# Kernel tuning notes

Measured on AMD Instinct MI355X. Metric: run time of the kernel, lower is better.

The kernel has to match this reference:

```python
import jax, jax.numpy as jnp
import numpy as np

B, S, IK, IV = 16, 2048, 3, 1
D = IK + IV          # input_size = 4
H = 256              # hidden_size
F = 512              # dim_feedforward
L = 2                # num_layers
EPS = 1e-5


def setup_inputs() -> dict:
    key = jax.random.key(0)
    ks = jax.random.split(key, 16)
    n = jax.random.normal
    inp = {
        'KEY': n(ks[0], (B, S, IK), jnp.float32),
        'VALUE': n(ks[1], (B, S, IV), jnp.float32),
        # per-layer kernel-attention projections (stacked on layer axis)
        'Wq': n(ks[2], (L, D, H), jnp.float32) * 0.1,
        'bq': jnp.zeros((L, H), jnp.float32),
        'Wk': n(ks[3], (L, D, H), jnp.float32) * 0.1,
        'bk': jnp.zeros((L, H), jnp.float32),
        'Wv': n(ks[4], (L, D, H), jnp.float32) * 0.1,
        'bv': jnp.zeros((L, H), jnp.float32),
        'Wo': n(ks[5], (L, H, D), jnp.float32) * 0.1,
        'bo': jnp.zeros((L, D), jnp.float32),
        'bw': jnp.ones((L,), jnp.float32),          # Gaussian kernel bandwidth
        # LayerNorm 1
        'g1': jnp.ones((L, D), jnp.float32),
        'be1': jnp.zeros((L, D), jnp.float32),
        # FFN
        'W1': n(ks[6], (L, D, F), jnp.float32) * 0.1,
        'b1': jnp.zeros((L, F), jnp.float32),
        'W2': n(ks[7], (L, F, D), jnp.float32) * 0.1,
        'b2': jnp.zeros((L, D), jnp.float32),
        # LayerNorm 2
        'g2': jnp.ones((L, D), jnp.float32),
        'be2': jnp.zeros((L, D), jnp.float32),
        # final fc: input_size -> input_v
        'Wfc': n(ks[8], (D, IV), jnp.float32) * 0.1,
        'bfc': jnp.zeros((IV,), jnp.float32),
    }
    return inp


def _layernorm(x, g, b):
    m = x.mean(-1, keepdims=True)
    v = ((x - m) ** 2).mean(-1, keepdims=True)
    return (x - m) * jax.lax.rsqrt(v + EPS) * g + b


def reference(KEY, VALUE, Wq, bq, Wk, bk, Wv, bv, Wo, bo, bw,
              g1, be1, W1, b1, W2, b2, g2, be2, Wfc, bfc):
    # positioning: concat coords and values -> [B, S, D]
    X = jnp.concatenate([KEY, VALUE], axis=-1)
    n_layers = Wq.shape[0]
    for i in range(n_layers):
        # Nadaraya-Watson Gaussian kernel attention (madsnn, type='nwd', kernel='gauss')
        Q = X @ Wq[i] + bq[i]                      # [B,S,H]
        K = X @ Wk[i] + bk[i]                      # [B,S,H]
        V = X @ Wv[i] + bv[i]                      # [B,S,H]
        # pairwise squared distances ||q-k||^2, [B,S,S]
        d2 = ((Q * Q).sum(-1)[:, :, None]
              + (K * K).sum(-1)[:, None, :]
              - 2.0 * jnp.einsum('bqh,bkh->bqk', Q, K))
        attn = jax.nn.softmax(-0.5 * d2 * (bw[i] ** 2), axis=-1)
        attn_out = jnp.einsum('bqk,bkh->bqh', attn, V) @ Wo[i] + bo[i]  # [B,S,D]
        # residual + LayerNorm + FFN + residual + LayerNorm (dropout = identity in eval)
        res = _layernorm(X + attn_out, g1[i], be1[i])
        ff = jax.nn.relu(res @ W1[i] + b1[i]) @ W2[i] + b2[i]
        X = _layernorm(res + ff, g2[i], be2[i])
    return X @ Wfc + bfc                            # [B,S,IV]
```

## Files before the change

### kernel.cpp

```cpp
#include <hip/hip_runtime.h>

#define BB 16
#define SS 2048
#define NTOK (BB*SS)
#define FF 512
#define EPSF 1e-5f

#if __has_builtin(__builtin_amdgcn_exp2f)
#define EXP2F(x) __builtin_amdgcn_exp2f(x)
#else
#define EXP2F(x) exp2f(x)
#endif

typedef float v2f __attribute__((ext_vector_type(2)));


__device__ __forceinline__ float wred64(float v) {
#pragma unroll
  for (int m = 32; m > 0; m >>= 1) v += __shfl_xor(v, m, 64);
  return v;
}


__global__ __launch_bounds__(256) void prep_kernel(
    const float* __restrict__ KEY, const float* __restrict__ VALUE,
    const float* __restrict__ Wq, const float* __restrict__ bq,
    const float* __restrict__ Wk, const float* __restrict__ bk,
    const float* __restrict__ Wv, const float* __restrict__ bv,
    const float* __restrict__ Wo, const float* __restrict__ bw,
    const float* __restrict__ W1, const float* __restrict__ b1,
    const float* __restrict__ W2,
    float* __restrict__ sm, float* __restrict__ w1t, float* __restrict__ X0)
{
  const int bid = blockIdx.x;
  if (bid < 128) {
    const int gq = bid*256 + threadIdx.x;
    *(float4*)(X0 + (size_t)gq*4) =
        make_float4(KEY[gq*3 + 0], KEY[gq*3 + 1], KEY[gq*3 + 2], VALUE[gq]);
    return;
  }
  const int i = bid - 128;
  if (threadIdx.x >= 64) return;
  const int lane = threadIdx.x;
  float m4[4][4] = {{0}}, gkk[4][4] = {{0}}, wvo[4][4] = {{0}};
  float akk[4] = {0}, bvo[4] = {0};
  float ck1 = 0.f, ck2 = 0.f;

  for (int h = lane; h < 256; h += 64) {
    float vq[4], vk[4], vv[4], wo4[4];
#pragma unroll
    for (int a = 0; a < 4; ++a) {
      vq[a]  = Wq[(i*4 + a)*256 + h];
      vk[a]  = Wk[(i*4 + a)*256 + h];
      vv[a]  = Wv[(i*4 + a)*256 + h];
      wo4[a] = Wo[(i*256 + h)*4 + a];
    }
    const float bqh = bq[i*256 + h], bkh = bk[i*256 + h], bvh = bv[i*256 + h];
#pragma unroll
    for (int a = 0; a < 4; ++a) {
#pragma unroll
      for (int c = 0; c < 4; ++c) {
        m4[a][c]  = fmaf(vq[a], vk[c], m4[a][c]);
        gkk[a][c] = fmaf(vk[a], vk[c], gkk[a][c]);
        wvo[a][c] = fmaf(vv[a], wo4[c], wvo[a][c]);
      }
      akk[a] = fmaf(vk[a], bqh - bkh, akk[a]);
      bvo[a] = fmaf(bvh, wo4[a], bvo[a]);
    }
    ck1 = fmaf(bqh, bkh, ck1);
    ck2 = fmaf(bkh, bkh, ck2);
  }
#pragma unroll
  for (int a = 0; a < 4; ++a) {
#pragma unroll
    for (int c = 0; c < 4; ++c) {
      m4[a][c]  = wred64(m4[a][c]);
      gkk[a][c] = wred64(gkk[a][c]);
      wvo[a][c] = wred64(wvo[a][c]);
    }
    akk[a] = wred64(akk[a]);
    bvo[a] = wred64(bvo[a]);
  }
  ck1 = wred64(ck1); ck2 = wred64(ck2);

  if (lane == 0) {
    const float bwv = bw[i];
    const float bw2 = bwv * bwv * 1.44269504088896f;
    float* s = sm + i*64;
#pragma unroll
    for (int a = 0; a < 4; ++a) {
#pragma unroll
      for (int c = 0; c < 4; ++c) {
        s[a*4+c]      = bw2 * m4[a][c];
        s[16 + a*4+c] = -0.5f * bw2 * gkk[a][c];
        s[32 + a*4+c] = wvo[a][c];
      }
      s[48+a] = bw2 * akk[a];
      s[52+a] = bvo[a];
    }
    s[56] = bw2 * (ck1 - 0.5f * ck2);
  }
  for (int f = lane; f < FF; f += 64) {
    float* rec = w1t + (i*FF + f)*12;
#pragma unroll
    for (int c = 0; c < 4; ++c) rec[c]   = W1[(i*4 + c)*FF + f];
#pragma unroll
    for (int c = 0; c < 4; ++c) rec[4+c] = W2[(i*FF + f)*4 + c];
    rec[8] = b1[i*FF + f];
    rec[9] = 0.f; rec[10] = 0.f; rec[11] = 0.f;
  }
}

__device__ __forceinline__ void compute_feat(const float x[4], const float* __restrict__ s,
                                             float* __restrict__ featrec)
{
  float P[4], VT[4], tk[4];
#pragma unroll
  for (int a = 0; a < 4; ++a) {
    P[a]  = fmaf(s[a*4+3], x[3], fmaf(s[a*4+2], x[2], fmaf(s[a*4+1], x[1], s[a*4+0]*x[0])));
    tk[a] = fmaf(s[16+a*4+3], x[3], fmaf(s[16+a*4+2], x[2], fmaf(s[16+a*4+1], x[1], s[16+a*4+0]*x[0])));
    VT[a] = s[52+a] + fmaf(s[32+3*4+a], x[3], fmaf(s[32+2*4+a], x[2], fmaf(s[32+1*4+a], x[1], s[32+0*4+a]*x[0])));
  }
  float R = s[56];
#pragma unroll
  for (int a = 0; a < 4; ++a) R = fmaf(tk[a] + s[48+a], x[a], R);
  float4* fp = (float4*)featrec;
  fp[0] = make_float4(P[0], P[1], P[2], P[3]);
  fp[1] = make_float4(VT[0], VT[1], VT[2], VT[3]);
  fp[2] = make_float4(R, 0.f, 0.f, 0.f);
}

__global__ __launch_bounds__(256) void attn_kernel(
    const float* __restrict__ X, const float* __restrict__ sm,
    float* __restrict__ part)
{
  __shared__ float smem[512*21];
  const int bid = blockIdx.x;
  const int b = bid >> 5;
  const int r = bid & 31;
  const int qg = r >> 3, kb = r & 7;
  const int qbase = (b << 11) + (qg << 9);
  const int kbase = (b << 11) + (kb << 8);
  const int tid = threadIdx.x;
  const int lane = tid & 63, wave = tid >> 6;

  {
    const float4 xk = *(const float4*)(X + (size_t)(kbase + tid)*4);
    float xr[4] = {xk.x, xk.y, xk.z, xk.w};
    float fr[12];
    compute_feat(xr, sm, fr);
    float* dst = smem + tid*12;
    ((float4*)dst)[0] = ((float4*)fr)[0];
    ((float4*)dst)[1] = ((float4*)fr)[1];
    dst[8] = fr[8];
  }

  v2f xq2[4][4], axy[8], azw[8], ad[4];
#pragma unroll
  for (int jp = 0; jp < 4; ++jp) {
    const float4 xa = *(const float4*)(X + (size_t)(qbase + (2*jp  )*64 + lane)*4);
    const float4 xb = *(const float4*)(X + (size_t)(qbase + (2*jp+1)*64 + lane)*4);
    xq2[jp][0] = v2f{xa.x, xb.x};
    xq2[jp][1] = v2f{xa.y, xb.y};
    xq2[jp][2] = v2f{xa.z, xb.z};
    xq2[jp][3] = v2f{xa.w, xb.w};
    ad[jp] = v2f{0.f, 0.f};
  }
#pragma unroll
  for (int j = 0; j < 8; ++j) { axy[j] = v2f{0.f, 0.f}; azw[j] = v2f{0.f, 0.f}; }
  __syncthreads();

  const float* kf = smem + wave*64*12;
#pragma unroll 2
  for (int k = 0; k < 64; ++k) {
    const float* kp = kf + k*12;
    const float4 P  = *(const float4*)kp;
    const float4 VT = *(const float4*)(kp + 4);
    const float R = kp[8];
    const v2f Rv  = v2f{R, R};
    const v2f Px  = v2f{P.x, P.x}, Py = v2f{P.y, P.y};
    const v2f Pz  = v2f{P.z, P.z}, Pw = v2f{P.w, P.w};
    const v2f Vxy = v2f{VT.x, VT.y}, Vzw = v2f{VT.z, VT.w};
#pragma unroll
    for (int jp = 0; jp < 4; ++jp) {
      v2f l = __builtin_elementwise_fma(xq2[jp][0], Px, Rv);
      l = __builtin_elementwise_fma(xq2[jp][1], Py, l);
      l = __builtin_elementwise_fma(xq2[jp][2], Pz, l);
      l = __builtin_elementwise_fma(xq2[jp][3], Pw, l);
      const float e0 = EXP2F(l.x);
      const float e1 = EXP2F(l.y);
      const v2f e0v = v2f{e0, e0}, e1v = v2f{e1, e1};
      axy[2*jp  ] = __builtin_elementwise_fma(e0v, Vxy, axy[2*jp  ]);
      azw[2*jp  ] = __builtin_elementwise_fma(e0v, Vzw, azw[2*jp  ]);
      axy[2*jp+1] = __builtin_elementwise_fma(e1v, Vxy, axy[2*jp+1]);
      azw[2*jp+1] = __builtin_elementwise_fma(e1v, Vzw, azw[2*jp+1]);
      ad[jp] += v2f{e0, e1};
    }
  }
  __syncthreads();
#pragma unroll
  for (int j = 0; j < 8; ++j) {
    float* rr = smem + (j*64 + lane)*21 + wave*5;
    rr[0] = axy[j].x; rr[1] = axy[j].y; rr[2] = azw[j].x;
    rr[3] = azw[j].y; rr[4] = (j & 1) ? ad[j>>1].y : ad[j>>1].x;
  }
  __syncthreads();
  float* pb = part + (size_t)kb * NTOK * 8;
#pragma unroll
  for (int t = 0; t < 2; ++t) {
    const int q = t*256 + tid;
    const float* rr = smem + q*21;
    float s0 = 0.f, s1 = 0.f, s2 = 0.f, s3 = 0.f, s4 = 0.f;
#pragma unroll
    for (int w = 0; w < 4; ++w) {
      s0 += rr[w*5+0]; s1 += rr[w*5+1]; s2 += rr[w*5+2];
      s3 += rr[w*5+3]; s4 += rr[w*5+4];
    }
    float* pp = pb + (size_t)(qbase + q)*8;
    *(float4*)pp = make_float4(s0, s1, s2, s3);
    pp[4] = s4;
  }
}

__device__ __forceinline__ void ln4(const float t[4], const float* __restrict__ g,
                                    const float* __restrict__ b, float r[4])
{
  const float m = 0.25f*(t[0]+t[1]+t[2]+t[3]);
  const float d0 = t[0]-m, d1 = t[1]-m, d2 = t[2]-m, d3 = t[3]-m;
  const float v = 0.25f*(d0*d0 + d1*d1 + d2*d2 + d3*d3);
  const float sc = rsqrtf(v + EPSF);
  r[0] = fmaf(d0*sc, g[0], b[0]);
  r[1] = fmaf(d1*sc, g[1], b[1]);
  r[2] = fmaf(d2*sc, g[2], b[2]);
  r[3] = fmaf(d3*sc, g[3], b[3]);
}

__global__ __launch_bounds__(512) void combine_kernel(
    const float* __restrict__ part, const float* __restrict__ Xin,
    const float* __restrict__ w1t,
    const float* __restrict__ bo, const float* __restrict__ g1, const float* __restrict__ be1,
    const float* __restrict__ b2v, const float* __restrict__ g2, const float* __restrict__ be2,
    float* __restrict__ Xout,
    const float* __restrict__ Wfc, const float* __restrict__ bfc,
    float* __restrict__ outp, int last)
{
  const int tok = threadIdx.x & 63, fc = threadIdx.x >> 6;
  const int gq = blockIdx.x*64 + tok;
  __shared__ float redp[8][64][5];
  __shared__ float ress[64][4];
  __shared__ float redf[8][64][4];

  {
    const float* pp = part + ((size_t)fc*NTOK + gq)*8;
    const float4 v = *(const float4*)pp;
    redp[fc][tok][0] = v.x; redp[fc][tok][1] = v.y;
    redp[fc][tok][2] = v.z; redp[fc][tok][3] = v.w;
    redp[fc][tok][4] = pp[4];
  }
  __syncthreads();

  if (fc == 0) {
    float acc[5] = {0,0,0,0,0};
#pragma unroll
    for (int k = 0; k < 8; ++k)
#pragma unroll
      for (int c = 0; c < 5; ++c) acc[c] += redp[k][tok][c];
    const float inv = 1.0f / acc[4];
    const float4 xv = *(const float4*)(Xin + (size_t)gq*4);
    float t[4];
    t[0] = xv.x + fmaf(acc[0], inv, bo[0]);
    t[1] = xv.y + fmaf(acc[1], inv, bo[1]);
    t[2] = xv.z + fmaf(acc[2], inv, bo[2]);
    t[3] = xv.w + fmaf(acc[3], inv, bo[3]);
    float r[4];
    ln4(t, g1, be1, r);
    ress[tok][0] = r[0]; ress[tok][1] = r[1]; ress[tok][2] = r[2]; ress[tok][3] = r[3];
  }
  __syncthreads();

  const float r0 = ress[tok][0], r1 = ress[tok][1], r2 = ress[tok][2], r3 = ress[tok][3];
  float fa[4] = {0,0,0,0};
  const float* wt = w1t + (size_t)fc*64*12;
#pragma unroll 4
  for (int f = 0; f < 64; ++f) {
    const float* rec = wt + f*12;
    const float4 w1r = *(const float4*)rec;
    const float4 w2r = *(const float4*)(rec + 4);
    const float b1f = rec[8];
    float h = fmaf(r3, w1r.w, fmaf(r2, w1r.z, fmaf(r1, w1r.y, fmaf(r0, w1r.x, b1f))));
    h = fmaxf(h, 0.f);
    fa[0] = fmaf(h, w2r.x, fa[0]);
    fa[1] = fmaf(h, w2r.y, fa[1]);
    fa[2] = fmaf(h, w2r.z, fa[2]);
    fa[3] = fmaf(h, w2r.w, fa[3]);
  }
  redf[fc][tok][0] = fa[0]; redf[fc][tok][1] = fa[1];
  redf[fc][tok][2] = fa[2]; redf[fc][tok][3] = fa[3];
  __syncthreads();

  if (fc == 0) {
    float t2[4];
#pragma unroll
    for (int c = 0; c < 4; ++c) {
      float s = b2v[c];
#pragma unroll
      for (int k = 0; k < 8; ++k) s += redf[k][tok][c];
      t2[c] = ress[tok][c] + s;
    }
    float y[4];
    ln4(t2, g2, be2, y);
    if (last) {
      outp[gq] = fmaf(y[3], Wfc[3], fmaf(y[2], Wfc[2], fmaf(y[1], Wfc[1], fmaf(y[0], Wfc[0], bfc[0]))));
    } else {
      *(float4*)(Xout + (size_t)gq*4) = make_float4(y[0], y[1], y[2], y[3]);
    }
  }
}

extern "C" void kernel_launch(void* const* d_in, const int* in_sizes, int n_in,
                              void* d_out, int out_size, void* d_ws, size_t ws_size,
                              hipStream_t stream)
{
  const float* KEY   = (const float*)d_in[0];
  const float* VALUE = (const float*)d_in[1];
  const float* Wq  = (const float*)d_in[2];
  const float* bq  = (const float*)d_in[3];
  const float* Wk  = (const float*)d_in[4];
  const float* bk  = (const float*)d_in[5];
  const float* Wv  = (const float*)d_in[6];
  const float* bv  = (const float*)d_in[7];
  const float* Wo  = (const float*)d_in[8];
  const float* bo  = (const float*)d_in[9];
  const float* bw  = (const float*)d_in[10];
  const float* g1  = (const float*)d_in[11];
  const float* be1 = (const float*)d_in[12];
  const float* W1  = (const float*)d_in[13];
  const float* b1  = (const float*)d_in[14];
  const float* W2  = (const float*)d_in[15];
  const float* b2  = (const float*)d_in[16];
  const float* g2  = (const float*)d_in[17];
  const float* be2 = (const float*)d_in[18];
  const float* Wfc = (const float*)d_in[19];
  const float* bfc = (const float*)d_in[20];
  float* out = (float*)d_out;

  float* w    = (float*)d_ws;
  float* sm   = w;
  float* w1t  = w + 128;
  float* X0   = w + 12416;
  float* X1   = w + 143488;
  float* part = w + 274560;

  prep_kernel<<<130, 256, 0, stream>>>(KEY, VALUE, Wq, bq, Wk, bk, Wv, bv, Wo, bw,
                                       W1, b1, W2, sm, w1t, X0);

  attn_kernel<<<512, 256, 0, stream>>>(X0, sm, part);
  combine_kernel<<<512, 512, 0, stream>>>(part, X0, w1t,
      bo, g1, be1, b2, g2, be2,
      X1, Wfc, bfc, out, 0);

  attn_kernel<<<512, 256, 0, stream>>>(X1, sm + 64, part);
  combine_kernel<<<512, 512, 0, stream>>>(part, X1, w1t + FF*12,
      bo + 4, g1 + 4, be1 + 4, b2 + 4, g2 + 4, be2 + 4,
      X0, Wfc, bfc, out, 1);
}
```

Baseline: 182.5 us.

## Halve attention query tile per block and pack FFN weights for paired-float math

The attention kernel now handles 256 queries per block instead of 512, doubling the grid to 1024 blocks and halving per-thread accumulator registers. Key features are now computed twice as often across blocks. Separately, the FFN weights are repacked into 24-float records covering two hidden units, so the combine kernel can run the FFN with packed two-wide FMAs. The aims are higher occupancy and better load balance in attention, and fewer instructions in the FFN loop.

Measured after the change: 184.1 us. No clear change (+0.9%).

```diff
diff --git a/kernel.cpp b/kernel.cpp
--- a/kernel.cpp
+++ b/kernel.cpp
@@ -100,14 +100,20 @@
     }
     s[56] = bw2 * (ck1 - 0.5f * ck2);
   }
-  for (int f = lane; f < FF; f += 64) {
-    float* rec = w1t + (i*FF + f)*12;
-#pragma unroll
-    for (int c = 0; c < 4; ++c) rec[c]   = W1[(i*4 + c)*FF + f];
-#pragma unroll
-    for (int c = 0; c < 4; ++c) rec[4+c] = W2[(i*FF + f)*4 + c];
-    rec[8] = b1[i*FF + f];
-    rec[9] = 0.f; rec[10] = 0.f; rec[11] = 0.f;
+  for (int fp = lane; fp < 256; fp += 64) {
+    const int f0 = 2*fp, f1 = 2*fp + 1;
+    float* rec = w1t + (i*256 + fp)*24;
+#pragma unroll
+    for (int c = 0; c < 4; ++c) {
+      rec[c*2 + 0] = W1[(i*4 + c)*FF + f0];
+      rec[c*2 + 1] = W1[(i*4 + c)*FF + f1];
+      rec[8 + c*2 + 0] = W2[((size_t)i*FF + f0)*4 + c];
+      rec[8 + c*2 + 1] = W2[((size_t)i*FF + f1)*4 + c];
+    }
+    rec[16] = b1[i*FF + f0];
+    rec[17] = b1[i*FF + f1];
+#pragma unroll
+    for (int c = 18; c < 24; ++c) rec[c] = 0.f;
   }
 }
 
@@ -134,12 +140,12 @@
     const float* __restrict__ X, const float* __restrict__ sm,
     float* __restrict__ part)
 {
-  __shared__ float smem[512*21];
+  __shared__ float smem[256*21];
   const int bid = blockIdx.x;
-  const int b = bid >> 5;
-  const int r = bid & 31;
+  const int b = bid >> 6;
+  const int r = bid & 63;
   const int qg = r >> 3, kb = r & 7;
-  const int qbase = (b << 11) + (qg << 9);
+  const int qbase = (b << 11) + (qg << 8);
   const int kbase = (b << 11) + (kb << 8);
   const int tid = threadIdx.x;
   const int lane = tid & 63, wave = tid >> 6;
@@ -155,9 +161,9 @@
     dst[8] = fr[8];
   }
 
-  v2f xq2[4][4], axy[8], azw[8], ad[4];
-#pragma unroll
-  for (int jp = 0; jp < 4; ++jp) {
+  v2f xq2[2][4], axy[4], azw[4], ad[2];
+#pragma unroll
+  for (int jp = 0; jp < 2; ++jp) {
     const float4 xa = *(const float4*)(X + (size_t)(qbase + (2*jp  )*64 + lane)*4);
     const float4 xb = *(const float4*)(X + (size_t)(qbase + (2*jp+1)*64 + lane)*4);
     xq2[jp][0] = v2f{xa.x, xb.x};
@@ -167,7 +173,7 @@
     ad[jp] = v2f{0.f, 0.f};
   }
 #pragma unroll
-  for (int j = 0; j < 8; ++j) { axy[j] = v2f{0.f, 0.f}; azw[j] = v2f{0.f, 0.f}; }
+  for (int j = 0; j < 4; ++j) { axy[j] = v2f{0.f, 0.f}; azw[j] = v2f{0.f, 0.f}; }
   __syncthreads();
 
   const float* kf = smem + wave*64*12;
@@ -182,7 +188,7 @@
     const v2f Pz  = v2f{P.z, P.z}, Pw = v2f{P.w, P.w};
     const v2f Vxy = v2f{VT.x, VT.y}, Vzw = v2f{VT.z, VT.w};
 #pragma unroll
-    for (int jp = 0; jp < 4; ++jp) {
+    for (int jp = 0; jp < 2; ++jp) {
       v2f l = __builtin_elementwise_fma(xq2[jp][0], Px, Rv);
       l = __builtin_elementwise_fma(xq2[jp][1], Py, l);
       l = __builtin_elementwise_fma(xq2[jp][2], Pz, l);
@@ -199,24 +205,21 @@
   }
   __syncthreads();
 #pragma unroll
-  for (int j = 0; j < 8; ++j) {
+  for (int j = 0; j < 4; ++j) {
     float* rr = smem + (j*64 + lane)*21 + wave*5;
     rr[0] = axy[j].x; rr[1] = axy[j].y; rr[2] = azw[j].x;
     rr[3] = azw[j].y; rr[4] = (j & 1) ? ad[j>>1].y : ad[j>>1].x;
   }
   __syncthreads();
-  float* pb = part + (size_t)kb * NTOK * 8;
-#pragma unroll
-  for (int t = 0; t < 2; ++t) {
-    const int q = t*256 + tid;
-    const float* rr = smem + q*21;
+  {
+    const float* rr = smem + tid*21;
     float s0 = 0.f, s1 = 0.f, s2 = 0.f, s3 = 0.f, s4 = 0.f;
 #pragma unroll
     for (int w = 0; w < 4; ++w) {
       s0 += rr[w*5+0]; s1 += rr[w*5+1]; s2 += rr[w*5+2];
       s3 += rr[w*5+3]; s4 += rr[w*5+4];
     }
-    float* pp = pb + (size_t)(qbase + q)*8;
+    float* pp = part + ((size_t)kb * NTOK + qbase + tid)*8;
     *(float4*)pp = make_float4(s0, s1, s2, s3);
     pp[4] = s4;
   }
@@ -278,24 +281,36 @@
   }
   __syncthreads();
 
-  const float r0 = ress[tok][0], r1 = ress[tok][1], r2 = ress[tok][2], r3 = ress[tok][3];
-  float fa[4] = {0,0,0,0};
-  const float* wt = w1t + (size_t)fc*64*12;
+  const v2f r0v = v2f{ress[tok][0], ress[tok][0]};
+  const v2f r1v = v2f{ress[tok][1], ress[tok][1]};
+  const v2f r2v = v2f{ress[tok][2], ress[tok][2]};
+  const v2f r3v = v2f{ress[tok][3], ress[tok][3]};
+  v2f f2[4];
+#pragma unroll
+  for (int c = 0; c < 4; ++c) f2[c] = v2f{0.f, 0.f};
+  const float* wt = w1t + (size_t)fc*32*24;
 #pragma unroll 4
-  for (int f = 0; f < 64; ++f) {
-    const float* rec = wt + f*12;
-    const float4 w1r = *(const float4*)rec;
-    const float4 w2r = *(const float4*)(rec + 4);
-    const float b1f = rec[8];
-    float h = fmaf(r3, w1r.w, fmaf(r2, w1r.z, fmaf(r1, w1r.y, fmaf(r0, w1r.x, b1f))));
-    h = fmaxf(h, 0.f);
-    fa[0] = fmaf(h, w2r.x, fa[0]);
-    fa[1] = fmaf(h, w2r.y, fa[1]);
-    fa[2] = fmaf(h, w2r.z, fa[2]);
-    fa[3] = fmaf(h, w2r.w, fa[3]);
-  }
-  redf[fc][tok][0] = fa[0]; redf[fc][tok][1] = fa[1];
-  redf[fc][tok][2] = fa[2]; redf[fc][tok][3] = fa[3];
+  for (int fp = 0; fp < 32; ++fp) {
+    const float* rec = wt + fp*24;
+    const float4 w1a = *(const float4*)rec;
+    const float4 w1b = *(const float4*)(rec + 4);
+    const float4 w2a = *(const float4*)(rec + 8);
+    const float4 w2b = *(const float4*)(rec + 12);
+    const v2f bv = *(const v2f*)(rec + 16);
+    v2f hv = __builtin_elementwise_fma(v2f{w1a.x, w1a.y}, r0v, bv);
+    hv = __builtin_elementwise_fma(v2f{w1a.z, w1a.w}, r1v, hv);
+    hv = __builtin_elementwise_fma(v2f{w1b.x, w1b.y}, r2v, hv);
+    hv = __builtin_elementwise_fma(v2f{w1b.z, w1b.w}, r3v, hv);
+    hv = __builtin_elementwise_max(hv, v2f{0.f, 0.f});
+    f2[0] = __builtin_elementwise_fma(hv, v2f{w2a.x, w2a.y}, f2[0]);
+    f2[1] = __builtin_elementwise_fma(hv, v2f{w2a.z, w2a.w}, f2[1]);
+    f2[2] = __builtin_elementwise_fma(hv, v2f{w2b.x, w2b.y}, f2[2]);
+    f2[3] = __builtin_elementwise_fma(hv, v2f{w2b.z, w2b.w}, f2[3]);
+  }
+  redf[fc][tok][0] = f2[0].x + f2[0].y;
+  redf[fc][tok][1] = f2[1].x + f2[1].y;
+  redf[fc][tok][2] = f2[2].x + f2[2].y;
+  redf[fc][tok][3] = f2[3].x + f2[3].y;
   __syncthreads();
 
   if (fc == 0) {
@@ -354,13 +369,13 @@
   prep_kernel<<<130, 256, 0, stream>>>(KEY, VALUE, Wq, bq, Wk, bk, Wv, bv, Wo, bw,
                                        W1, b1, W2, sm, w1t, X0);
 
-  attn_kernel<<<512, 256, 0, stream>>>(X0, sm, part);
+  attn_kernel<<<1024, 256, 0, stream>>>(X0, sm, part);
   combine_kernel<<<512, 512, 0, stream>>>(part, X0, w1t,
       bo, g1, be1, b2, g2, be2,
       X1, Wfc, bfc, out, 0);
 
-  attn_kernel<<<512, 256, 0, stream>>>(X1, sm + 64, part);
-  combine_kernel<<<512, 512, 0, stream>>>(part, X1, w1t + FF*12,
+  attn_kernel<<<1024, 256, 0, stream>>>(X1, sm + 64, part);
+  combine_kernel<<<512, 512, 0, stream>>>(part, X1, w1t + 256*24,
       bo + 4, g1 + 4, be1 + 4, b2 + 4, g2 + 4, be2 + 4,
       X0, Wfc, bfc, out, 1);
 }
```
